# Performance work log

Measured on AMD Instinct MI355X. Metric: run time of the kernel, lower is better.

## Reference

```python
import jax, jax.numpy as jnp
import numpy as np

H_IMG, W_IMG = 1024, 1280
MAX_ITER = 3
DAMPING = 1e-6
DIST_THR = 0.2
NORM_THR = float(np.cos(np.deg2rad(20.0)))


def setup_inputs() -> dict:
    key = jax.random.key(0)
    k1, k2, k3, k4 = jax.random.split(key, 4)
    H, W = H_IMG, W_IMG
    fx = fy = 1000.0
    cx, cy = (W - 1) / 2.0, (H - 1) / 2.0
    K = jnp.array([[fx, 0.0, cx], [0.0, fy, cy], [0.0, 0.0, 1.0]], dtype=jnp.float32)
    # backproject a random depth map so vertex maps are geometrically consistent with K
    depth = 0.5 + 2.5 * jax.random.uniform(k1, (H, W), dtype=jnp.float32)
    vv, uu = jnp.meshgrid(jnp.arange(H, dtype=jnp.float32), jnp.arange(W, dtype=jnp.float32), indexing='ij')
    vertex_t0 = jnp.stack([(uu - cx) / fx * depth, (vv - cy) / fy * depth, depth], axis=-1)
    n = jax.random.normal(k2, (H, W, 3), dtype=jnp.float32) * 0.1 + jnp.array([0.0, 0.0, -1.0], jnp.float32)
    normal_t0 = n / jnp.linalg.norm(n, axis=-1, keepdims=True)
    # frame 1 = slightly perturbed frame 0 (realistic small-motion ICP)
    vertex_t1 = vertex_t0 + 0.002 * jax.random.normal(k3, (H, W, 3), dtype=jnp.float32)
    n1 = normal_t0 + 0.01 * jax.random.normal(k4, (H, W, 3), dtype=jnp.float32)
    normal_t1 = n1 / jnp.linalg.norm(n1, axis=-1, keepdims=True)
    pose10 = jnp.eye(4, dtype=jnp.float32).at[:3, 3].set(jnp.array([0.005, -0.003, 0.002], jnp.float32))
    return {
        'pose10': pose10,
        'vertex_t0': vertex_t0.astype(jnp.float32),
        'vertex_t1': vertex_t1.astype(jnp.float32),
        'normal_t0': normal_t0.astype(jnp.float32),
        'normal_t1': normal_t1.astype(jnp.float32),
        'K': K,
    }


def _skew3(w):
    o = jnp.zeros((), w.dtype)
    return jnp.array([[o, -w[2], w[1]], [w[2], o, -w[0]], [-w[1], w[0], o]])


def _exp_se3(xi):
    w, v = xi[:3], xi[3:6]
    wh = _skew3(w)
    wh2 = wh @ wh
    theta = jnp.linalg.norm(w)
    eps = 1e-8
    ts = jnp.maximum(theta, eps)  # safe denominator
    sin_t, cos_t = jnp.sin(ts), jnp.cos(ts)
    eye3 = jnp.eye(3, dtype=xi.dtype)
    e_w_big = eye3 + wh * (sin_t / ts) + wh2 * ((1.0 - cos_t) / ts ** 2)
    j_big = eye3 + ((1.0 - cos_t) / ts ** 2) * wh + ((ts - sin_t) / ts ** 3) * wh2
    small = theta <= eps
    e_w = jnp.where(small, eye3, e_w_big)
    j = jnp.where(small, eye3, j_big)
    return jnp.eye(4, dtype=xi.dtype).at[:3, :3].set(e_w).at[:3, 3].set(j @ v)


def _warp_nearest(feat, u, v):
    # grid_sample(mode='nearest', padding='border', align_corners=True) with
    # the module's normalization reduces to nearest-pixel gather at (v,u), clamped.
    H, W, _ = feat.shape
    ui = jnp.clip(jnp.round(u), 0, W - 1).astype(jnp.int32)
    vi = jnp.clip(jnp.round(v), 0, H - 1).astype(jnp.int32)
    return feat[vi, ui]  # (H,W,C)


def _icp_step(pose, vertex0, vertex1, normal0, normal1, mask0, K):
    R, t = pose[:3, :3], pose[:3, 3]
    H, W, _ = vertex0.shape
    p = vertex0 @ R.T + t          # vertex0_to1, (H,W,3)
    n0 = normal0 @ R.T             # normal0_to1
    fx, fy, cx, cy = K[0, 0], K[1, 1], K[0, 2], K[1, 2]
    z = p[..., 2]
    u = p[..., 0] / z * fx + cx
    v = p[..., 1] / z * fy + cy
    inview = (u > 0) & (u < W - 1) & (v > 0) & (v < H - 1)
    rv1 = _warp_nearest(vertex1, u, v)
    rn1 = _warp_nearest(normal1, u, v)
    mask1 = rv1[..., -1] > 0.0
    diff = p - rv1
    normal_ok = jnp.sum(n0 * rn1, axis=-1) > NORM_THR
    res = jnp.sum(rn1 * diff, axis=-1)           # (H,W)
    # -n^T skew(p) == cross(p, n)
    J = jnp.concatenate([jnp.cross(p, rn1), rn1], axis=-1)  # (H,W,6)
    occ = (~inview) | (jnp.linalg.norm(diff, axis=-1) > DIST_THR)
    invalid = occ | (~mask0) | (~mask1) | (~normal_ok)
    J = jnp.where(invalid[..., None], 0.0, J).reshape(-1, 6)
    r = jnp.where(invalid, 0.0, res).reshape(-1)
    JtJ = J.T @ J                                 # (6,6)
    JtR = J.T @ r                                 # (6,)
    Hm = JtJ + jnp.trace(JtJ) * DAMPING * jnp.eye(6, dtype=JtJ.dtype)
    xi = -(jnp.linalg.inv(Hm) @ JtR)
    return _exp_se3(xi) @ pose, ~invalid


def reference(pose10, vertex_t0, vertex_t1, normal_t0, normal_t1, K):
    mask0 = vertex_t0[..., -1] > 0.0
    pose = pose10
    valid = None
    for _ in range(MAX_ITER):
        pose, valid = _icp_step(pose, vertex_t0, vertex_t1, normal_t0, normal_t1, mask0, K)
    H, W = vertex_t0.shape[:2]
    valid_ratio = valid.astype(jnp.float32).sum() / H / W
    return pose, valid_ratio
```

## Files before the change

kernel.cpp:

```cpp
#include <hip/hip_runtime.h>
#include <math.h>

#define H_IMG 1024
#define W_IMG 1280
#define NPIX (H_IMG * W_IMG)
#define NQUAD (NPIX / 4)
#define RBLOCKS 256
#define RTPB 128
#define NWAVES (RTPB / 64)
#define QPT (NQUAD / (RBLOCKS * RTPB))
#define NACC 28
#define NORM_THR 0.93969262f
#define DIST_THR2 0.04f
#define DAMPING 1e-6

#define PART_DOUBLES (RBLOCKS * NACC)

typedef __attribute__((ext_vector_type(4))) float f4;

__global__ __launch_bounds__(256) void icp_init(const float* __restrict__ pose_in,
                                                double* __restrict__ ws) {
    const int i = threadIdx.x;
    if (i < 16) ws[i] = (double)pose_in[i];
    for (int k = i; k < PART_DOUBLES; k += 256) ws[16 + k] = 0.0;
    if (i == 0) *(unsigned*)(ws + 16 + PART_DOUBLES) = 0u;
}

__device__ void solve_and_update(const double* tot, double* pose_ws,
                                 float* out, int write_out) {
    double JtJ[6][6];
    {
        int k = 0;
        for (int i = 0; i < 6; ++i)
            for (int j = i; j < 6; ++j) { JtJ[i][j] = tot[k]; JtJ[j][i] = tot[k]; ++k; }
    }
    double tr = 0.0;
    for (int i = 0; i < 6; ++i) tr += JtJ[i][i];

    double A[6][7];
    for (int i = 0; i < 6; ++i) {
        for (int j = 0; j < 6; ++j) A[i][j] = JtJ[i][j] + (i == j ? tr * DAMPING : 0.0);
        A[i][6] = -tot[21 + i];
    }
    for (int c = 0; c < 6; ++c) {
        int piv = c; double mx = fabs(A[c][c]);
        for (int r = c + 1; r < 6; ++r) {
            double ar = fabs(A[r][c]);
            if (ar > mx) { mx = ar; piv = r; }
        }
        if (piv != c) for (int j = 0; j < 7; ++j) { double tmp = A[c][j]; A[c][j] = A[piv][j]; A[piv][j] = tmp; }
        double d = A[c][c]; if (d == 0.0) d = 1e-30;
        for (int r = c + 1; r < 6; ++r) {
            double f = A[r][c] / d;
            for (int j = c; j < 7; ++j) A[r][j] -= f * A[c][j];
        }
    }
    double xi[6];
    for (int i = 5; i >= 0; --i) {
        double s = A[i][6];
        for (int j = i + 1; j < 6; ++j) s -= A[i][j] * xi[j];
        double d = A[i][i]; if (d == 0.0) d = 1e-30;
        xi[i] = s / d;
    }

    const double w0 = xi[0], w1 = xi[1], w2 = xi[2];
    const double v0 = xi[3], v1 = xi[4], v2 = xi[5];
    double wh[3][3] = { {0.0, -w2, w1}, {w2, 0.0, -w0}, {-w1, w0, 0.0} };
    double wh2[3][3];
    for (int i = 0; i < 3; ++i)
        for (int j = 0; j < 3; ++j) {
            double s = 0.0;
            for (int k = 0; k < 3; ++k) s += wh[i][k] * wh[k][j];
            wh2[i][j] = s;
        }
    const double theta = sqrt(w0 * w0 + w1 * w1 + w2 * w2);
    const double eps = 1e-8;
    const double ts = (theta > eps) ? theta : eps;
    const double st = sin(ts), ct = cos(ts);
    const double cA = st / ts;
    const double cB = (1.0 - ct) / (ts * ts);
    const double cC = (ts - st) / (ts * ts * ts);
    const bool small = (theta <= eps);

    double ew[3][3], Jm[3][3];
    for (int i = 0; i < 3; ++i)
        for (int j = 0; j < 3; ++j) {
            double eye = (i == j) ? 1.0 : 0.0;
            ew[i][j] = small ? eye : (eye + cA * wh[i][j] + cB * wh2[i][j]);
            Jm[i][j] = small ? eye : (eye + cB * wh[i][j] + cC * wh2[i][j]);
        }
    double Jv[3];
    for (int i = 0; i < 3; ++i) Jv[i] = Jm[i][0] * v0 + Jm[i][1] * v1 + Jm[i][2] * v2;

    double T[16] = { ew[0][0], ew[0][1], ew[0][2], Jv[0],
                     ew[1][0], ew[1][1], ew[1][2], Jv[1],
                     ew[2][0], ew[2][1], ew[2][2], Jv[2],
                     0.0, 0.0, 0.0, 1.0 };
    double P[16];
    for (int i = 0; i < 16; ++i) P[i] = pose_ws[i];
    double NP[16];
    for (int i = 0; i < 4; ++i)
        for (int j = 0; j < 4; ++j) {
            double s = 0.0;
            for (int k = 0; k < 4; ++k) s += T[i * 4 + k] * P[k * 4 + j];
            NP[i * 4 + j] = s;
        }
    for (int i = 0; i < 16; ++i) pose_ws[i] = NP[i];

    if (write_out) {
        for (int i = 0; i < 16; ++i) out[i] = (float)NP[i];
        out[16] = (float)(tot[27] / (double)NPIX);
    }
}

__global__ __launch_bounds__(RTPB, 1) void icp_fused(
    const float* __restrict__ vert0, const float* __restrict__ vert1,
    const float* __restrict__ norm0, const float* __restrict__ norm1,
    const float* __restrict__ Kmat, double* __restrict__ ws,
    float* __restrict__ out, int write_out)
{
    const double* pose = ws;
    double* part = ws + 16;
    unsigned* counter = (unsigned*)(ws + 16 + PART_DOUBLES);

    const float R00 = (float)pose[0],  R01 = (float)pose[1],  R02 = (float)pose[2],  t0 = (float)pose[3];
    const float R10 = (float)pose[4],  R11 = (float)pose[5],  R12 = (float)pose[6],  t1 = (float)pose[7];
    const float R20 = (float)pose[8],  R21 = (float)pose[9],  R22 = (float)pose[10], t2 = (float)pose[11];
    const float fx = Kmat[0], cx = Kmat[2], fy = Kmat[4], cy = Kmat[5];

    float a[NACC];
#pragma unroll
    for (int k = 0; k < NACC; ++k) a[k] = 0.0f;

    const int tid0 = blockIdx.x * RTPB + threadIdx.x;
    const f4* v0q = (const f4*)vert0;
    const f4* n0q = (const f4*)norm0;

    f4 cA0, cA1, cA2, cB0, cB1, cB2;
    {
        const int q = tid0;
        cA0 = v0q[q * 3 + 0]; cA1 = v0q[q * 3 + 1]; cA2 = v0q[q * 3 + 2];
        cB0 = n0q[q * 3 + 0]; cB1 = n0q[q * 3 + 1]; cB2 = n0q[q * 3 + 2];
    }

#pragma unroll
    for (int i = 0; i < QPT; ++i) {
        const float vx[4] = {cA0.x, cA0.w, cA1.z, cA2.y};
        const float vy[4] = {cA0.y, cA1.x, cA1.w, cA2.z};
        const float vz[4] = {cA0.z, cA1.y, cA2.x, cA2.w};
        const float nx[4] = {cB0.x, cB0.w, cB1.z, cB2.y};
        const float ny[4] = {cB0.y, cB1.x, cB1.w, cB2.z};
        const float nz[4] = {cB0.z, cB1.y, cB2.x, cB2.w};

        float px[4], py[4], pz[4], nrx[4], nry[4], nrz[4];
        bool inview[4];
        int wb[4];
#pragma unroll
        for (int p = 0; p < 4; ++p) {
            px[p] = R00 * vx[p] + R01 * vy[p] + R02 * vz[p] + t0;
            py[p] = R10 * vx[p] + R11 * vy[p] + R12 * vz[p] + t1;
            pz[p] = R20 * vx[p] + R21 * vy[p] + R22 * vz[p] + t2;
            nrx[p] = R00 * nx[p] + R01 * ny[p] + R02 * nz[p];
            nry[p] = R10 * nx[p] + R11 * ny[p] + R12 * nz[p];
            nrz[p] = R20 * nx[p] + R21 * ny[p] + R22 * nz[p];
            const float u = px[p] / pz[p] * fx + cx;
            const float v = py[p] / pz[p] * fy + cy;
            inview[p] = (u > 0.0f) && (u < (float)(W_IMG - 1)) &&
                        (v > 0.0f) && (v < (float)(H_IMG - 1));
            const float uf = fminf(fmaxf(rintf(u), 0.0f), (float)(W_IMG - 1));
            const float vf = fminf(fmaxf(rintf(v), 0.0f), (float)(H_IMG - 1));
            wb[p] = ((int)vf * W_IMG + (int)uf) * 3;
        }

        float r1x[4], r1y[4], r1z[4], m1x[4], m1y[4], m1z[4];
#pragma unroll
        for (int p = 0; p < 4; ++p) {
            r1x[p] = vert1[wb[p]]; r1y[p] = vert1[wb[p] + 1]; r1z[p] = vert1[wb[p] + 2];
            m1x[p] = norm1[wb[p]]; m1y[p] = norm1[wb[p] + 1]; m1z[p] = norm1[wb[p] + 2];
        }

        f4 nA0, nA1, nA2, nB0, nB1, nB2;
        if (i + 1 < QPT) {
            const int q = tid0 + (i + 1) * (RBLOCKS * RTPB);
            nA0 = v0q[q * 3 + 0]; nA1 = v0q[q * 3 + 1]; nA2 = v0q[q * 3 + 2];
            nB0 = n0q[q * 3 + 0]; nB1 = n0q[q * 3 + 1]; nB2 = n0q[q * 3 + 2];
        }

#pragma unroll
        for (int p = 0; p < 4; ++p) {
            const float dx = px[p] - r1x[p], dy = py[p] - r1y[p], dz = pz[p] - r1z[p];
            const bool mask0 = vz[p] > 0.0f;
            const bool mask1 = r1z[p] > 0.0f;
            const bool normal_ok =
                (nrx[p] * m1x[p] + nry[p] * m1y[p] + nrz[p] * m1z[p]) > NORM_THR;
            const float d2 = dx * dx + dy * dy + dz * dz;
            const bool occ = (!inview[p]) || (d2 > DIST_THR2);
            const bool valid = (!occ) && mask0 && mask1 && normal_ok;

            if (valid) {
                const float res = m1x[p] * dx + m1y[p] * dy + m1z[p] * dz;
                float J[6];
                J[0] = py[p] * m1z[p] - pz[p] * m1y[p];
                J[1] = pz[p] * m1x[p] - px[p] * m1z[p];
                J[2] = px[p] * m1y[p] - py[p] * m1x[p];
                J[3] = m1x[p]; J[4] = m1y[p]; J[5] = m1z[p];
                int k = 0;
#pragma unroll
                for (int ii = 0; ii < 6; ++ii)
#pragma unroll
                    for (int jj = ii; jj < 6; ++jj) a[k++] += J[ii] * J[jj];
#pragma unroll
                for (int ii = 0; ii < 6; ++ii) a[21 + ii] += J[ii] * res;
                a[27] += 1.0f;
            }
        }

        if (i + 1 < QPT) {
            cA0 = nA0; cA1 = nA1; cA2 = nA2;
            cB0 = nB0; cB1 = nB1; cB2 = nB2;
        }
    }

#pragma unroll
    for (int k = 0; k < NACC; ++k) {
        float val = a[k];
        for (int off = 32; off > 0; off >>= 1) val += __shfl_down(val, off, 64);
        a[k] = val;
    }

    __shared__ float sh[NWAVES][NACC];
    const int lane = threadIdx.x & 63;
    const int wid  = threadIdx.x >> 6;
    if (lane == 0) {
#pragma unroll
        for (int k = 0; k < NACC; ++k) sh[wid][k] = a[k];
    }
    __syncthreads();

    const unsigned tid = threadIdx.x;
    if (tid < NACC) {
        double s = 0.0;
#pragma unroll
        for (int w = 0; w < NWAVES; ++w) s += (double)sh[w][tid];
        __hip_atomic_store(&part[blockIdx.x * NACC + (int)tid], s,
                           __ATOMIC_RELAXED, __HIP_MEMORY_SCOPE_AGENT);
    }
    __syncthreads();

    __shared__ bool amLast;
    if (tid == 0) {
        __threadfence();
        unsigned prev = atomicAdd(counter, 1u);
        amLast = (prev == gridDim.x - 1);
    }
    __syncthreads();

    if (amLast) {
        __threadfence();
        __shared__ double red[4][NACC];
        __shared__ double tot[NACC];
        const int k = (int)tid % NACC;
        const int g = (int)tid / NACC;
        if (tid < 4 * NACC) {
            double s = 0.0;
#pragma unroll
            for (int b = 0; b < RBLOCKS / 4; ++b) {
                const int blk = g + b * 4;
                s += __hip_atomic_load(&part[blk * NACC + k],
                                       __ATOMIC_RELAXED, __HIP_MEMORY_SCOPE_AGENT);
            }
            red[g][k] = s;
        }
        __syncthreads();
        if (tid < NACC) {
            double s = 0.0;
#pragma unroll
            for (int g2 = 0; g2 < 4; ++g2) s += red[g2][tid];
            tot[tid] = s;
        }
        __syncthreads();
        if (tid == 0) {
            solve_and_update(tot, ws, out, write_out);
            atomicExch(counter, 0u);
        }
    }
}

extern "C" void kernel_launch(void* const* d_in, const int* in_sizes, int n_in,
                              void* d_out, int out_size, void* d_ws, size_t ws_size,
                              hipStream_t stream) {
    const float* pose10 = (const float*)d_in[0];
    const float* vert0  = (const float*)d_in[1];
    const float* vert1  = (const float*)d_in[2];
    const float* norm0  = (const float*)d_in[3];
    const float* norm1  = (const float*)d_in[4];
    const float* Kmat   = (const float*)d_in[5];
    float* out = (float*)d_out;
    double* ws = (double*)d_ws;

    icp_init<<<1, 256, 0, stream>>>(pose10, ws);
    for (int it = 0; it < 3; ++it) {
        icp_fused<<<RBLOCKS, RTPB, 0, stream>>>(vert0, vert1, norm0, norm1,
                                                Kmat, ws, out, it == 2 ? 1 : 0);
    }
}
```

Baseline: 207.9 us.

## Pack frame-1 vertex and normal into 32-byte records for gather

A prep kernel repacks vertex_t1 and normal_t1 into an interleaved 32-byte-per-pixel buffer in the workspace. Each ICP iteration can then fetch the projected correspondence with two aligned 16-byte loads instead of scattered AoS float3 reads from two arrays. The change also doubles threads per block and swizzles the block-to-data mapping, presumably to spread memory traffic more evenly. In exchange it adds a full read-and-write pass over frame 1 and needs a large workspace, falling back to the old path when the workspace is too small.

Result: faster. 189.8 us (-8.7%).

```diff
diff --git a/kernel.cpp b/kernel.cpp
--- a/kernel.cpp
+++ b/kernel.cpp
@@ -6,7 +6,7 @@
 #define NPIX (H_IMG * W_IMG)
 #define NQUAD (NPIX / 4)
 #define RBLOCKS 256
-#define RTPB 128
+#define RTPB 256
 #define NWAVES (RTPB / 64)
 #define QPT (NQUAD / (RBLOCKS * RTPB))
 #define NACC 28
@@ -15,6 +15,9 @@
 #define DAMPING 1e-6
 
 #define PART_DOUBLES (RBLOCKS * NACC)
+#define PACK_BYTE_OFF 65536
+#define PACK_BYTES ((size_t)NPIX * 32)
+#define WS_NEEDED (PACK_BYTE_OFF + PACK_BYTES)
 
 typedef __attribute__((ext_vector_type(4))) float f4;
 
@@ -24,6 +27,44 @@
     if (i < 16) ws[i] = (double)pose_in[i];
     for (int k = i; k < PART_DOUBLES; k += 256) ws[16 + k] = 0.0;
     if (i == 0) *(unsigned*)(ws + 16 + PART_DOUBLES) = 0u;
+}
+
+__global__ __launch_bounds__(RTPB) void icp_prep(
+    const float* __restrict__ pose_in,
+    const float* __restrict__ vert1, const float* __restrict__ norm1,
+    double* __restrict__ ws)
+{
+    const int tid = threadIdx.x;
+    if (blockIdx.x == 0) {
+        if (tid < 16) ws[tid] = (double)pose_in[tid];
+        if (tid == 16) *(unsigned*)(ws + 16 + PART_DOUBLES) = 0u;
+    }
+
+    f4* pk = (f4*)((char*)ws + PACK_BYTE_OFF);
+    const f4* v1q = (const f4*)vert1;
+    const f4* n1q = (const f4*)norm1;
+    const int t0 = blockIdx.x * RTPB + tid;
+
+#pragma unroll
+    for (int i = 0; i < QPT; ++i) {
+        const int q = t0 + i * (RBLOCKS * RTPB);
+        const f4 A0 = v1q[q * 3 + 0], A1 = v1q[q * 3 + 1], A2 = v1q[q * 3 + 2];
+        const f4 B0 = n1q[q * 3 + 0], B1 = n1q[q * 3 + 1], B2 = n1q[q * 3 + 2];
+        const float vx[4] = {A0.x, A0.w, A1.z, A2.y};
+        const float vy[4] = {A0.y, A1.x, A1.w, A2.z};
+        const float vz[4] = {A0.z, A1.y, A2.x, A2.w};
+        const float nx[4] = {B0.x, B0.w, B1.z, B2.y};
+        const float ny[4] = {B0.y, B1.x, B1.w, B2.z};
+        const float nz[4] = {B0.z, B1.y, B2.x, B2.w};
+#pragma unroll
+        for (int p = 0; p < 4; ++p) {
+            const int r = q * 4 + p;
+            f4 g0 = {vx[p], vy[p], vz[p], nx[p]};
+            f4 g1 = {ny[p], nz[p], 0.0f, 0.0f};
+            pk[r * 2 + 0] = g0;
+            pk[r * 2 + 1] = g1;
+        }
+    }
 }
 
 __device__ void solve_and_update(const double* tot, double* pose_ws,
@@ -113,15 +154,196 @@
     }
 }
 
-__global__ __launch_bounds__(RTPB, 1) void icp_fused(
+__device__ __forceinline__ void reduce_and_finish(
+    float a[NACC], double* ws, float* out, int write_out)
+{
+    double* part = ws + 16;
+    unsigned* counter = (unsigned*)(ws + 16 + PART_DOUBLES);
+
+#pragma unroll
+    for (int k = 0; k < NACC; ++k) {
+        float val = a[k];
+        for (int off = 32; off > 0; off >>= 1) val += __shfl_down(val, off, 64);
+        a[k] = val;
+    }
+
+    __shared__ float sh[NWAVES][NACC];
+    const int lane = threadIdx.x & 63;
+    const int wid  = threadIdx.x >> 6;
+    if (lane == 0) {
+#pragma unroll
+        for (int k = 0; k < NACC; ++k) sh[wid][k] = a[k];
+    }
+    __syncthreads();
+
+    const unsigned tid = threadIdx.x;
+    if (tid < NACC) {
+        double s = 0.0;
+#pragma unroll
+        for (int w = 0; w < NWAVES; ++w) s += (double)sh[w][tid];
+        __hip_atomic_store(&part[blockIdx.x * NACC + (int)tid], s,
+                           __ATOMIC_RELAXED, __HIP_MEMORY_SCOPE_AGENT);
+    }
+    __syncthreads();
+
+    __shared__ bool amLast;
+    if (tid == 0) {
+        __threadfence();
+        unsigned prev = atomicAdd(counter, 1u);
+        amLast = (prev == gridDim.x - 1);
+    }
+    __syncthreads();
+
+    if (amLast) {
+        __threadfence();
+        __shared__ double red[8][NACC];
+        __shared__ double tot[NACC];
+        const int k = (int)tid % NACC;
+        const int g = (int)tid / NACC;
+        if (tid < 8 * NACC) {
+            double s = 0.0;
+#pragma unroll
+            for (int b = 0; b < RBLOCKS / 8; ++b) {
+                const int blk = g + b * 8;
+                s += __hip_atomic_load(&part[blk * NACC + k],
+                                       __ATOMIC_RELAXED, __HIP_MEMORY_SCOPE_AGENT);
+            }
+            red[g][k] = s;
+        }
+        __syncthreads();
+        if (tid < NACC) {
+            double s = 0.0;
+#pragma unroll
+            for (int g2 = 0; g2 < 8; ++g2) s += red[g2][tid];
+            tot[tid] = s;
+        }
+        __syncthreads();
+        if (tid == 0) {
+            solve_and_update(tot, ws, out, write_out);
+            atomicExch(counter, 0u);
+        }
+    }
+}
+
+__global__ __launch_bounds__(RTPB, 1) void icp_fused_pk(
+    const float* __restrict__ vert0, const float* __restrict__ norm0,
+    const float* __restrict__ Kmat, double* __restrict__ ws,
+    float* __restrict__ out, int write_out)
+{
+    const double* pose = ws;
+    const f4* pk = (const f4*)((const char*)ws + PACK_BYTE_OFF);
+
+    const float R00 = (float)pose[0],  R01 = (float)pose[1],  R02 = (float)pose[2],  t0 = (float)pose[3];
+    const float R10 = (float)pose[4],  R11 = (float)pose[5],  R12 = (float)pose[6],  t1 = (float)pose[7];
+    const float R20 = (float)pose[8],  R21 = (float)pose[9],  R22 = (float)pose[10], t2 = (float)pose[11];
+    const float fx = Kmat[0], cx = Kmat[2], fy = Kmat[4], cy = Kmat[5];
+
+    float a[NACC];
+#pragma unroll
+    for (int k = 0; k < NACC; ++k) a[k] = 0.0f;
+
+    const int sbid = (blockIdx.x & 7) * 32 + (blockIdx.x >> 3);
+    const int tid0 = sbid * RTPB + threadIdx.x;
+    const f4* v0q = (const f4*)vert0;
+    const f4* n0q = (const f4*)norm0;
+
+    f4 cA0, cA1, cA2, cB0, cB1, cB2;
+    {
+        const int q = tid0;
+        cA0 = v0q[q * 3 + 0]; cA1 = v0q[q * 3 + 1]; cA2 = v0q[q * 3 + 2];
+        cB0 = n0q[q * 3 + 0]; cB1 = n0q[q * 3 + 1]; cB2 = n0q[q * 3 + 2];
+    }
+
+#pragma unroll
+    for (int i = 0; i < QPT; ++i) {
+        const float vx[4] = {cA0.x, cA0.w, cA1.z, cA2.y};
+        const float vy[4] = {cA0.y, cA1.x, cA1.w, cA2.z};
+        const float vz[4] = {cA0.z, cA1.y, cA2.x, cA2.w};
+        const float nx[4] = {cB0.x, cB0.w, cB1.z, cB2.y};
+        const float ny[4] = {cB0.y, cB1.x, cB1.w, cB2.z};
+        const float nz[4] = {cB0.z, cB1.y, cB2.x, cB2.w};
+
+        float px[4], py[4], pz[4], nrx[4], nry[4], nrz[4];
+        bool inview[4];
+        int ridx[4];
+#pragma unroll
+        for (int p = 0; p < 4; ++p) {
+            px[p] = R00 * vx[p] + R01 * vy[p] + R02 * vz[p] + t0;
+            py[p] = R10 * vx[p] + R11 * vy[p] + R12 * vz[p] + t1;
+            pz[p] = R20 * vx[p] + R21 * vy[p] + R22 * vz[p] + t2;
+            nrx[p] = R00 * nx[p] + R01 * ny[p] + R02 * nz[p];
+            nry[p] = R10 * nx[p] + R11 * ny[p] + R12 * nz[p];
+            nrz[p] = R20 * nx[p] + R21 * ny[p] + R22 * nz[p];
+            const float u = px[p] / pz[p] * fx + cx;
+            const float v = py[p] / pz[p] * fy + cy;
+            inview[p] = (u > 0.0f) && (u < (float)(W_IMG - 1)) &&
+                        (v > 0.0f) && (v < (float)(H_IMG - 1));
+            const float uf = fminf(fmaxf(rintf(u), 0.0f), (float)(W_IMG - 1));
+            const float vf = fminf(fmaxf(rintf(v), 0.0f), (float)(H_IMG - 1));
+            ridx[p] = (int)vf * W_IMG + (int)uf;
+        }
+
+        f4 g0[4], g1[4];
+#pragma unroll
+        for (int p = 0; p < 4; ++p) {
+            g0[p] = pk[ridx[p] * 2 + 0];
+            g1[p] = pk[ridx[p] * 2 + 1];
+        }
+
+        f4 nA0, nA1, nA2, nB0, nB1, nB2;
+        if (i + 1 < QPT) {
+            const int q = tid0 + (i + 1) * (RBLOCKS * RTPB);
+            nA0 = v0q[q * 3 + 0]; nA1 = v0q[q * 3 + 1]; nA2 = v0q[q * 3 + 2];
+            nB0 = n0q[q * 3 + 0]; nB1 = n0q[q * 3 + 1]; nB2 = n0q[q * 3 + 2];
+        }
+
+#pragma unroll
+        for (int p = 0; p < 4; ++p) {
+            const float r1x = g0[p].x, r1y = g0[p].y, r1z = g0[p].z;
+            const float m1x = g0[p].w, m1y = g1[p].x, m1z = g1[p].y;
+            const float dx = px[p] - r1x, dy = py[p] - r1y, dz = pz[p] - r1z;
+            const bool mask0 = vz[p] > 0.0f;
+            const bool mask1 = r1z > 0.0f;
+            const bool normal_ok =
+                (nrx[p] * m1x + nry[p] * m1y + nrz[p] * m1z) > NORM_THR;
+            const float d2 = dx * dx + dy * dy + dz * dz;
+            const bool occ = (!inview[p]) || (d2 > DIST_THR2);
+            const bool valid = (!occ) && mask0 && mask1 && normal_ok;
+
+            if (valid) {
+                const float res = m1x * dx + m1y * dy + m1z * dz;
+                float J[6];
+                J[0] = py[p] * m1z - pz[p] * m1y;
+                J[1] = pz[p] * m1x - px[p] * m1z;
+                J[2] = px[p] * m1y - py[p] * m1x;
+                J[3] = m1x; J[4] = m1y; J[5] = m1z;
+                int k = 0;
+#pragma unroll
+                for (int ii = 0; ii < 6; ++ii)
+#pragma unroll
+                    for (int jj = ii; jj < 6; ++jj) a[k++] += J[ii] * J[jj];
+#pragma unroll
+                for (int ii = 0; ii < 6; ++ii) a[21 + ii] += J[ii] * res;
+                a[27] += 1.0f;
+            }
+        }
+
+        if (i + 1 < QPT) {
+            cA0 = nA0; cA1 = nA1; cA2 = nA2;
+            cB0 = nB0; cB1 = nB1; cB2 = nB2;
+        }
+    }
+
+    reduce_and_finish(a, ws, out, write_out);
+}
+
+__global__ __launch_bounds__(RTPB, 1) void icp_fused_dg(
     const float* __restrict__ vert0, const float* __restrict__ vert1,
     const float* __restrict__ norm0, const float* __restrict__ norm1,
     const float* __restrict__ Kmat, double* __restrict__ ws,
     float* __restrict__ out, int write_out)
 {
     const double* pose = ws;
-    double* part = ws + 16;
-    unsigned* counter = (unsigned*)(ws + 16 + PART_DOUBLES);
 
     const float R00 = (float)pose[0],  R01 = (float)pose[1],  R02 = (float)pose[2],  t0 = (float)pose[3];
     const float R10 = (float)pose[4],  R11 = (float)pose[5],  R12 = (float)pose[6],  t1 = (float)pose[7];
@@ -132,7 +354,8 @@
 #pragma unroll
     for (int k = 0; k < NACC; ++k) a[k] = 0.0f;
 
-    const int tid0 = blockIdx.x * RTPB + threadIdx.x;
+    const int sbid = (blockIdx.x & 7) * 32 + (blockIdx.x >> 3);
+    const int tid0 = sbid * RTPB + threadIdx.x;
     const f4* v0q = (const f4*)vert0;
     const f4* n0q = (const f4*)norm0;
 
@@ -221,69 +444,7 @@
         }
     }
 
-#pragma unroll
-    for (int k = 0; k < NACC; ++k) {
-        float val = a[k];
-        for (int off = 32; off > 0; off >>= 1) val += __shfl_down(val, off, 64);
-        a[k] = val;
-    }
-
-    __shared__ float sh[NWAVES][NACC];
-    const int lane = threadIdx.x & 63;
-    const int wid  = threadIdx.x >> 6;
-    if (lane == 0) {
-#pragma unroll
-        for (int k = 0; k < NACC; ++k) sh[wid][k] = a[k];
-    }
-    __syncthreads();
-
-    const unsigned tid = threadIdx.x;
-    if (tid < NACC) {
-        double s = 0.0;
-#pragma unroll
-        for (int w = 0; w < NWAVES; ++w) s += (double)sh[w][tid];
-        __hip_atomic_store(&part[blockIdx.x * NACC + (int)tid], s,
-                           __ATOMIC_RELAXED, __HIP_MEMORY_SCOPE_AGENT);
-    }
-    __syncthreads();
-
-    __shared__ bool amLast;
-    if (tid == 0) {
-        __threadfence();
-        unsigned prev = atomicAdd(counter, 1u);
-        amLast = (prev == gridDim.x - 1);
-    }
-    __syncthreads();
-
-    if (amLast) {
-        __threadfence();
-        __shared__ double red[4][NACC];
-        __shared__ double tot[NACC];
-        const int k = (int)tid % NACC;
-        const int g = (int)tid / NACC;
-        if (tid < 4 * NACC) {
-            double s = 0.0;
-#pragma unroll
-            for (int b = 0; b < RBLOCKS / 4; ++b) {
-                const int blk = g + b * 4;
-                s += __hip_atomic_load(&part[blk * NACC + k],
-                                       __ATOMIC_RELAXED, __HIP_MEMORY_SCOPE_AGENT);
-            }
-            red[g][k] = s;
-        }
-        __syncthreads();
-        if (tid < NACC) {
-            double s = 0.0;
-#pragma unroll
-            for (int g2 = 0; g2 < 4; ++g2) s += red[g2][tid];
-            tot[tid] = s;
-        }
-        __syncthreads();
-        if (tid == 0) {
-            solve_and_update(tot, ws, out, write_out);
-            atomicExch(counter, 0u);
-        }
-    }
+    reduce_and_finish(a, ws, out, write_out);
 }
 
 extern "C" void kernel_launch(void* const* d_in, const int* in_sizes, int n_in,
@@ -298,9 +459,17 @@
     float* out = (float*)d_out;
     double* ws = (double*)d_ws;
 
-    icp_init<<<1, 256, 0, stream>>>(pose10, ws);
-    for (int it = 0; it < 3; ++it) {
-        icp_fused<<<RBLOCKS, RTPB, 0, stream>>>(vert0, vert1, norm0, norm1,
-                                                Kmat, ws, out, it == 2 ? 1 : 0);
-    }
-}
+    if (ws_size >= WS_NEEDED) {
+        icp_prep<<<RBLOCKS, RTPB, 0, stream>>>(pose10, vert1, norm1, ws);
+        for (int it = 0; it < 3; ++it) {
+            icp_fused_pk<<<RBLOCKS, RTPB, 0, stream>>>(vert0, norm0, Kmat, ws,
+                                                       out, it == 2 ? 1 : 0);
+        }
+    } else {
+        icp_init<<<1, 256, 0, stream>>>(pose10, ws);
+        for (int it = 0; it < 3; ++it) {
+            icp_fused_dg<<<RBLOCKS, RTPB, 0, stream>>>(vert0, vert1, norm0, norm1,
+                                                       Kmat, ws, out, it == 2 ? 1 : 0);
+        }
+    }
+}
```
